# Performance work log

Hardware: AMD Instinct MI355X
Metric: run time of the kernel (lower is better)

## Reference

```python
import jax, jax.numpy as jnp
import numpy as np

WS = (7, 7, 7)          # window size (S, H, W)
NUM_HEADS = 6
DIM = 192
B_, NW = 128, 32        # total windows, windows per image (mask dim)
N = WS[0] * WS[1] * WS[2]  # 343 tokens per window


def _relative_position_index():
    # Faithful replica of the torch __init__ logic (incl. indexing='xy' and
    # the 3*W1-1 / 2*W1-1 multipliers).
    cs = np.arange(WS[0]); ch = np.arange(WS[1]); cw = np.arange(WS[2])
    coords = np.stack(np.meshgrid(cs, ch, cw, indexing='xy'))  # (3, Wh, Ws, Ww)
    cf = coords.reshape(3, -1)                                  # (3, N)
    rel = cf[:, :, None] - cf[:, None, :]                       # (3, N, N)
    rel = rel.transpose(1, 2, 0).astype(np.int64)               # (N, N, 3)
    rel[:, :, 0] += WS[0] - 1
    rel[:, :, 1] += WS[1] - 1
    rel[:, :, 2] += WS[2] - 1
    rel[:, :, 0] *= 3 * WS[1] - 1
    rel[:, :, 1] *= 2 * WS[1] - 1
    return rel.sum(-1)                                          # (N, N) int


def setup_inputs() -> dict:
    key = jax.random.key(0)
    ks = jax.random.split(key, 6)
    C = DIM
    x = jax.random.normal(ks[0], (B_, N, C), dtype=jnp.float32)
    mask = jax.random.normal(ks[1], (NW, N, N), dtype=jnp.float32)
    qkv_w = jax.random.normal(ks[2], (3 * C, C), dtype=jnp.float32) * 0.02
    qkv_b = jnp.zeros((3 * C,), dtype=jnp.float32)
    proj_w = jax.random.normal(ks[3], (C, C), dtype=jnp.float32) * 0.02
    proj_b = jnp.zeros((C,), dtype=jnp.float32)
    table_len = (2 * WS[0] - 1) * (2 * WS[1] - 1) * (2 * WS[2] - 1)
    rpb_table = jax.random.normal(ks[4], (table_len, NUM_HEADS), dtype=jnp.float32) * 0.02
    rel_index = jnp.asarray(_relative_position_index(), dtype=jnp.int32)
    return {"x": x, "mask": mask, "qkv_w": qkv_w, "qkv_b": qkv_b,
            "proj_w": proj_w, "proj_b": proj_b, "rpb_table": rpb_table,
            "rel_index": rel_index}


def reference(x, mask, qkv_w, qkv_b, proj_w, proj_b, rpb_table, rel_index):
    B, n, C = x.shape
    H = NUM_HEADS
    hd = C // H
    scale = hd ** (-0.5)
    qkv = x @ qkv_w.T + qkv_b                      # (B, N, 3C)
    qkv = qkv.reshape(B, n, 3, H, hd).transpose(2, 0, 3, 1, 4)  # (3, B, H, N, hd)
    q, k, v = qkv[0] * scale, qkv[1], qkv[2]
    attn = jnp.einsum('bhnd,bhmd->bhnm', q, k)     # (B, H, N, N)
    bias = rpb_table[rel_index.reshape(-1)].reshape(n, n, H)
    attn = attn + bias.transpose(2, 0, 1)[None]    # (B, H, N, N)
    nW = mask.shape[0]
    attn = attn.reshape(B // nW, nW, H, n, n) + mask[None, :, None]
    attn = jax.nn.softmax(attn.reshape(B, H, n, n), axis=-1)
    out = jnp.einsum('bhnm,bhmd->bhnd', attn, v)   # (B, H, N, hd)
    out = out.transpose(0, 2, 1, 3).reshape(B, n, C)
    return out @ proj_w.T + proj_b
```

## Files before the change

kernel.cpp:

```cpp
#include <hip/hip_runtime.h>
#include <hip/hip_fp16.h>
#include <hip/hip_bf16.h>
#include <stdint.h>

#define WN 343
#define NH 6
#define HD 32
#define CD 192
#define NB 128
#define NWM 32
#define BMROW 352
#define BMSLICE (11*16*BMROW)
#define BMKC (16*BMROW)
#define LOG2E 1.4426950408889634f

typedef __attribute__((ext_vector_type(8))) short short8;
typedef __attribute__((ext_vector_type(4))) float f32x4;

__device__ __forceinline__ unsigned short f2bf(float f) {
  union { float f; uint32_t u; } v; v.f = f;
  uint32_t r = v.u + 0x7fffu + ((v.u >> 16) & 1u);
  return (unsigned short)(r >> 16);
}

__device__ __forceinline__ uint32_t pk2bf(float a, float b) {
  __hip_bfloat162 h = __float22bfloat162_rn(make_float2(a, b));
  return *(uint32_t*)&h;
}

__device__ __forceinline__ uint32_t pkh2(float a, float b) {
  __half2 h; h.x = __float2half(a); h.y = __float2half(b);
  return *(uint32_t*)&h;
}

__global__ __launch_bounds__(256) void prep_kernel(
    const float* __restrict__ wq, const float* __restrict__ wp,
    unsigned short* __restrict__ wqb, unsigned short* __restrict__ wpb,
    const int* __restrict__ rel, const float* __restrict__ rpb,
    const float* __restrict__ mask, uint32_t* __restrict__ bP,
    uint32_t* __restrict__ mP) {
  __shared__ float M[352][33];
  const int bid = blockIdx.x;
  if (bid < 66 + 352) {
    const bool isBias = (bid < 66);
    const int sub = isBias ? bid : bid - 66;
    const int grp = sub / 11;
    const int kc = sub - grp * 11;
    const int k0 = kc * 32;
    const float* mw = mask + (size_t)grp * (WN * WN);
    for (int idx = threadIdx.x; idx < 352 * 32; idx += 256) {
      int n = idx >> 5, k = idx & 31;
      float v;
      if (isBias) {
        int nc = (n < WN) ? n : (WN - 1);
        v = (k0 + k < WN) ? rpb[rel[nc * WN + k0 + k] * NH + grp] * LOG2E
                          : -30000.0f;
      } else {
        v = (n < WN && k0 + k < WN) ? mw[n * WN + k0 + k] * LOG2E : 0.0f;
      }
      M[n][k] = v;
    }
    __syncthreads();
    uint32_t* outp = (isBias ? bP : mP) + (size_t)grp * BMSLICE + (size_t)kc * BMKC;
#pragma unroll
    for (int quad = 0; quad < 4; ++quad) {
#pragma unroll
      for (int j = 0; j < 2; ++j) {
        int n = threadIdx.x + 256 * j;
        if (n < 352) {
          uint4 o;
          o.x = pkh2(M[n][quad * 8 + 0], M[n][quad * 8 + 4]);
          o.y = pkh2(M[n][quad * 8 + 1], M[n][quad * 8 + 5]);
          o.z = pkh2(M[n][quad * 8 + 2], M[n][quad * 8 + 6]);
          o.w = pkh2(M[n][quad * 8 + 3], M[n][quad * 8 + 7]);
          *(uint4*)(outp + ((size_t)quad * 352 + n) * 4) = o;
        }
      }
    }
    return;
  }
  const int NWQ = 3 * CD * CD;
  const int NWP = CD * CD;
  int i4 = ((bid - 418) * 256 + threadIdx.x) * 4;
  const float* src; unsigned short* dst; int off;
  if (i4 < NWQ) { src = wq; dst = wqb; off = i4; }
  else if (i4 < NWQ + NWP) { src = wp; dst = wpb; off = i4 - NWQ; }
  else return;
  f32x4 v = *(const f32x4*)(src + off);
  union { uint2 u2; uint32_t d[2]; } o;
  o.d[0] = pk2bf(v[0], v[1]);
  o.d[1] = pk2bf(v[2], v[3]);
  *(uint2*)(dst + off) = o.u2;
}

__global__ __launch_bounds__(256) void qkv_kernel(
    const float* __restrict__ x, const unsigned short* __restrict__ wqb,
    const float* __restrict__ bvec,
    unsigned short* __restrict__ qb, unsigned short* __restrict__ kb,
    unsigned short* __restrict__ vb) {
  __shared__ __align__(16) unsigned short Xs[128][40];
  __shared__ __align__(16) unsigned short Ws[192][40];
  const int tid = threadIdx.x;
  const int wave = tid >> 6, lane = tid & 63;
  const int quad = lane >> 4, c = lane & 15;
  const int m0 = blockIdx.x * 128;
  const int s = blockIdx.y;
  const int n0 = s * 192;

  f32x4 acc[2][12];
#pragma unroll
  for (int i = 0; i < 2; ++i)
#pragma unroll
    for (int j = 0; j < 12; ++j) acc[i][j] = (f32x4){0.f, 0.f, 0.f, 0.f};

  for (int kt = 0; kt < 6; ++kt) {
    const int k0 = kt * 32;
#pragma unroll
    for (int it = 0; it < 2; ++it) {
      int tq = tid + it * 256;
      int r = tq >> 2, ch = tq & 3;
      const float* src = x + (size_t)(m0 + r) * CD + k0 + ch * 8;
      f32x4 a = *(const f32x4*)src;
      f32x4 b = *(const f32x4*)(src + 4);
      union { short8 v8; uint32_t d[4]; } pk;
      pk.d[0] = pk2bf(a[0], a[1]);
      pk.d[1] = pk2bf(a[2], a[3]);
      pk.d[2] = pk2bf(b[0], b[1]);
      pk.d[3] = pk2bf(b[2], b[3]);
      *(short8*)&Xs[r][ch * 8] = pk.v8;
    }
#pragma unroll
    for (int it = 0; it < 3; ++it) {
      int r = it * 64 + (tid >> 2), ch = tid & 3;
      *(short8*)&Ws[r][ch * 8] =
          *(const short8*)(wqb + (size_t)(n0 + r) * CD + k0 + ch * 8);
    }
    __syncthreads();
    short8 af0 = *(const short8*)&Xs[wave * 32 + c][quad * 8];
    short8 af1 = *(const short8*)&Xs[wave * 32 + 16 + c][quad * 8];
#pragma unroll
    for (int j = 0; j < 12; ++j) {
      short8 bfr = *(const short8*)&Ws[j * 16 + c][quad * 8];
      acc[0][j] = __builtin_amdgcn_mfma_f32_16x16x32_bf16(af0, bfr, acc[0][j], 0, 0, 0);
      acc[1][j] = __builtin_amdgcn_mfma_f32_16x16x32_bf16(af1, bfr, acc[1][j], 0, 0, 0);
    }
    __syncthreads();
  }

  const float qscale = 0.25503486f;
  unsigned short* dst = (s == 0) ? qb : ((s == 1) ? kb : vb);
  const float scl = (s == 0) ? qscale : 1.0f;
  unsigned short (*Lh0)[40] = (unsigned short (*)[40])&Xs[0][0];
  unsigned short (*Lh1)[40] = (unsigned short (*)[40])&Ws[0][0];
  for (int hh = 0; hh < 3; ++hh) {
    __syncthreads();
#pragma unroll
    for (int jj = 0; jj < 4; ++jj) {
      int j = hh * 4 + jj;
      int hl = jj >> 1;
      int dd = (jj & 1) * 16 + c;
      float bn = bvec[n0 + j * 16 + c];
      unsigned short (*L)[40] = hl ? Lh1 : Lh0;
#pragma unroll
      for (int i = 0; i < 2; ++i)
#pragma unroll
        for (int r = 0; r < 4; ++r) {
          int m = wave * 32 + i * 16 + quad * 4 + r;
          L[m][dd] = f2bf((acc[i][j][r] + bn) * scl);
        }
    }
    __syncthreads();
    const int m = tid & 127;
    const int hl = tid >> 7;
    const int M = m0 + m;
    const int b = M / WN;
    const int tok = M - b * WN;
    const int h = hh * 2 + hl;
    unsigned short (*L)[40] = hl ? Lh1 : Lh0;
    unsigned short* drow = dst + (((size_t)b * NH + h) * WN + tok) * HD;
#pragma unroll
    for (int t2 = 0; t2 < 4; ++t2) {
      int d0 = t2 * 8;
      *(short8*)&drow[d0] = *(const short8*)&L[m][d0];
    }
  }
}

__global__ __launch_bounds__(512) void attn_kernel(
    const unsigned short* __restrict__ qb, const unsigned short* __restrict__ kb,
    const unsigned short* __restrict__ vb, const uint32_t* __restrict__ biasP,
    const uint32_t* __restrict__ maskP, unsigned short* __restrict__ ob) {
  __shared__ __align__(16) unsigned short Ks[352][40];
  __shared__ __align__(16) unsigned short Vt[HD][360];
  const int bid = blockIdx.x;
  const int job = (bid & 7) * 96 + (bid >> 3);
  const int wdx = job / 24;
  const int inner = job - wdx * 24;
  const int h = inner >> 2;
  const int b = (inner & 3) * 32 + wdx;
  const int tid = threadIdx.x;
  const int wave = tid >> 6, lane = tid & 63;
  const int quad = lane >> 4, c = lane & 15;
  const size_t base = ((size_t)b * NH + h) * (WN * HD);
  const unsigned short* q = qb + base;
  const unsigned short* k = kb + base;
  const unsigned short* v = vb + base;
  const uint32_t* bP = biasP + (size_t)h * BMSLICE;
  const uint32_t* mP = maskP + (size_t)wdx * BMSLICE;

  for (int t = tid; t < WN * 4; t += 512) {
    int r = t >> 2, ch = t & 3;
    int kk = r & 31;
    int row = (r & ~31) + 16 * ((kk >> 2) & 1) + 4 * (kk >> 3) + (kk & 3);
    *(short8*)&Ks[row][ch * 8] = *(const short8*)(k + r * HD + ch * 8);
  }
  for (int t = tid; t < 9 * 32; t += 512) {
    int kg = WN + (t >> 5);
    int kk = kg & 31;
    int row = (kg & ~31) + 16 * ((kk >> 2) & 1) + 4 * (kk >> 3) + (kk & 3);
    Ks[row][t & 31] = 0;
  }
  for (int t = tid; t < WN; t += 512) {
#pragma unroll
    for (int ch = 0; ch < 4; ++ch) {
      short8 vv = *(const short8*)(v + t * HD + ch * 8);
#pragma unroll
      for (int j = 0; j < 8; ++j) Vt[ch * 8 + j][t] = vv[j];
    }
  }
  for (int t = tid; t < 9 * 32; t += 512) {
    Vt[t & 31][WN + (t >> 5)] = 0;
  }
  __syncthreads();

  for (int qt = wave; qt < 22; qt += 8) {
    const int q0 = qt * 16;
    int qr = q0 + c; if (qr > WN - 1) qr = WN - 1;
    const short8 qf = *(const short8*)(q + qr * HD + quad * 8);
    const uint32_t* bRow = bP + ((size_t)quad * 352 + q0 + c) * 4;
    const uint32_t* mRow = mP + ((size_t)quad * 352 + q0 + c) * 4;

    f32x4 o0 = (f32x4){0.f, 0.f, 0.f, 0.f}, o1 = (f32x4){0.f, 0.f, 0.f, 0.f};
    float l = 0.f;
#pragma unroll
    for (int kc = 0; kc < 11; ++kc) {
      uint4 bw4 = *(const uint4*)(bRow + (size_t)kc * BMKC);
      uint4 mw4 = *(const uint4*)(mRow + (size_t)kc * BMKC);
      f32x4 cc0, cc1;
      {
        __half2 s2; float2 f;
        s2 = __hadd2(*(__half2*)&bw4.x, *(__half2*)&mw4.x);
        f = __half22float2(s2); cc0[0] = f.x; cc1[0] = f.y;
        s2 = __hadd2(*(__half2*)&bw4.y, *(__half2*)&mw4.y);
        f = __half22float2(s2); cc0[1] = f.x; cc1[1] = f.y;
        s2 = __hadd2(*(__half2*)&bw4.z, *(__half2*)&mw4.z);
        f = __half22float2(s2); cc0[2] = f.x; cc1[2] = f.y;
        s2 = __hadd2(*(__half2*)&bw4.w, *(__half2*)&mw4.w);
        f = __half22float2(s2); cc0[3] = f.x; cc1[3] = f.y;
      }
      const int k0 = kc * 32;
      short8 kf0 = *(const short8*)&Ks[k0 + c][quad * 8];
      short8 kf1 = *(const short8*)&Ks[k0 + 16 + c][quad * 8];
      f32x4 s0 = __builtin_amdgcn_mfma_f32_16x16x32_bf16(kf0, qf, cc0, 0, 0, 0);
      f32x4 s1 = __builtin_amdgcn_mfma_f32_16x16x32_bf16(kf1, qf, cc1, 0, 0, 0);
      float p0 = __builtin_amdgcn_exp2f(s0[0]), p1 = __builtin_amdgcn_exp2f(s0[1]);
      float p2 = __builtin_amdgcn_exp2f(s0[2]), p3 = __builtin_amdgcn_exp2f(s0[3]);
      float p4 = __builtin_amdgcn_exp2f(s1[0]), p5 = __builtin_amdgcn_exp2f(s1[1]);
      float p6 = __builtin_amdgcn_exp2f(s1[2]), p7 = __builtin_amdgcn_exp2f(s1[3]);
      l += (p0 + p1 + p2 + p3) + (p4 + p5 + p6 + p7);
      union { short8 v8; uint32_t d[4]; } pf;
      pf.d[0] = pk2bf(p0, p1);
      pf.d[1] = pk2bf(p2, p3);
      pf.d[2] = pk2bf(p4, p5);
      pf.d[3] = pk2bf(p6, p7);
      short8 vf0 = *(const short8*)&Vt[c][k0 + quad * 8];
      short8 vf1 = *(const short8*)&Vt[16 + c][k0 + quad * 8];
      o0 = __builtin_amdgcn_mfma_f32_16x16x32_bf16(pf.v8, vf0, o0, 0, 0, 0);
      o1 = __builtin_amdgcn_mfma_f32_16x16x32_bf16(pf.v8, vf1, o1, 0, 0, 0);
    }
    l += __shfl_xor(l, 16);
    l += __shfl_xor(l, 32);

#pragma unroll
    for (int r = 0; r < 4; ++r) {
      int n = q0 + quad * 4 + r;
      if (n < WN) {
        float lq = __shfl(l, quad * 4 + r, 16);
        float inv = 1.0f / lq;
        size_t orow = ((size_t)b * WN + n) * CD + h * HD;
        ob[orow + c] = f2bf(o0[r] * inv);
        ob[orow + 16 + c] = f2bf(o1[r] * inv);
      }
    }
  }
}

__global__ __launch_bounds__(256) void proj_kernel(
    const unsigned short* __restrict__ ob, const unsigned short* __restrict__ wpb,
    const float* __restrict__ bvec, float* __restrict__ out) {
  __shared__ __align__(16) unsigned short Xs[64][40];
  __shared__ __align__(16) unsigned short Ws[192][40];
  const int tid = threadIdx.x;
  const int wave = tid >> 6, lane = tid & 63;
  const int quad = lane >> 4, c = lane & 15;
  const int m0 = blockIdx.x * 64;

  f32x4 acc[12];
#pragma unroll
  for (int j = 0; j < 12; ++j) acc[j] = (f32x4){0.f, 0.f, 0.f, 0.f};

  for (int kt = 0; kt < 6; ++kt) {
    const int k0 = kt * 32;
    {
      int r = tid >> 2, ch = tid & 3;
      *(short8*)&Xs[r][ch * 8] =
          *(const short8*)(ob + (size_t)(m0 + r) * CD + k0 + ch * 8);
    }
#pragma unroll
    for (int it = 0; it < 3; ++it) {
      int r = it * 64 + (tid >> 2), ch = tid & 3;
      *(short8*)&Ws[r][ch * 8] =
          *(const short8*)(wpb + (size_t)r * CD + k0 + ch * 8);
    }
    __syncthreads();
    short8 af = *(const short8*)&Xs[wave * 16 + c][quad * 8];
#pragma unroll
    for (int j = 0; j < 12; ++j) {
      short8 bfr = *(const short8*)&Ws[j * 16 + c][quad * 8];
      acc[j] = __builtin_amdgcn_mfma_f32_16x16x32_bf16(af, bfr, acc[j], 0, 0, 0);
    }
    __syncthreads();
  }

#pragma unroll
  for (int j = 0; j < 12; ++j) {
    int col = j * 16 + c;
    float bn = bvec[col];
#pragma unroll
    for (int r = 0; r < 4; ++r) {
      int m = m0 + wave * 16 + quad * 4 + r;
      out[(size_t)m * CD + col] = acc[j][r] + bn;
    }
  }
}

extern "C" void kernel_launch(void* const* d_in, const int* in_sizes, int n_in,
                              void* d_out, int out_size, void* d_ws, size_t ws_size,
                              hipStream_t stream) {
  const float* x      = (const float*)d_in[0];
  const float* mask   = (const float*)d_in[1];
  const float* qkv_w  = (const float*)d_in[2];
  const float* qkv_b  = (const float*)d_in[3];
  const float* proj_w = (const float*)d_in[4];
  const float* proj_b = (const float*)d_in[5];
  const float* rpb    = (const float*)d_in[6];
  const int*   rel    = (const int*)d_in[7];
  float* out = (float*)d_out;

  char* ws = (char*)d_ws;
  uint32_t* biasP = (uint32_t*)ws;
  size_t off = 1486848;
  uint32_t* maskP = (uint32_t*)(ws + off); off += 7929856;
  unsigned short* qb = (unsigned short*)(ws + off); off += 16859136;
  unsigned short* kb = (unsigned short*)(ws + off); off += 16859136;
  unsigned short* vb = (unsigned short*)(ws + off); off += 16859136;
  unsigned short* obuf = (unsigned short*)(ws + off); off += 16859136;
  unsigned short* wqb = (unsigned short*)(ws + off); off += 221184;
  unsigned short* wpb = (unsigned short*)(ws + off); off += 73728;

  hipLaunchKernelGGL(prep_kernel, dim3(418 + 144), dim3(256), 0, stream,
                     qkv_w, proj_w, wqb, wpb, rel, rpb, mask, biasP, maskP);
  hipLaunchKernelGGL(qkv_kernel, dim3(343, 3), dim3(256), 0, stream,
                     x, wqb, qkv_b, qb, kb, vb);
  hipLaunchKernelGGL(attn_kernel, dim3(NH * NB), dim3(512), 0, stream,
                     qb, kb, vb, biasP, maskP, obuf);
  hipLaunchKernelGGL(proj_kernel, dim3(686), dim3(256), 0, stream,
                     obuf, wpb, proj_b, out);
}
```

Measured before the change: 219.8 us.

## Stage full activation rows in LDS and stream weights from global in QKV/proj GEMMs

The QKV kernel now uses 64-row tiles. It loads and converts each tile's full 192-column slice of x to bf16 in LDS once, then loops over all three Q/K/V outputs inside one block. Before, x was reread and reconverted for each of three grid-y slices. Both QKV and projection kernels now read weight fragments directly from global memory (relying on cache) instead of staging them in LDS, which removes the per-k-step syncthreads. The cost is more global or L2 weight traffic per block, and a serial 3-way loop per block with smaller row tiles.

Measured after the change: 287.0 us. 1.31x slower.

```diff
diff --git a/kernel.cpp b/kernel.cpp
--- a/kernel.cpp
+++ b/kernel.cpp
@@ -98,90 +98,75 @@
     const float* __restrict__ bvec,
     unsigned short* __restrict__ qb, unsigned short* __restrict__ kb,
     unsigned short* __restrict__ vb) {
-  __shared__ __align__(16) unsigned short Xs[128][40];
-  __shared__ __align__(16) unsigned short Ws[192][40];
+  __shared__ __align__(16) unsigned short Xall[64][200];
+  __shared__ __align__(16) unsigned short Lh0[64][40];
+  __shared__ __align__(16) unsigned short Lh1[64][40];
   const int tid = threadIdx.x;
   const int wave = tid >> 6, lane = tid & 63;
   const int quad = lane >> 4, c = lane & 15;
-  const int m0 = blockIdx.x * 128;
-  const int s = blockIdx.y;
-  const int n0 = s * 192;
-
-  f32x4 acc[2][12];
-#pragma unroll
-  for (int i = 0; i < 2; ++i)
-#pragma unroll
-    for (int j = 0; j < 12; ++j) acc[i][j] = (f32x4){0.f, 0.f, 0.f, 0.f};
-
-  for (int kt = 0; kt < 6; ++kt) {
-    const int k0 = kt * 32;
-#pragma unroll
-    for (int it = 0; it < 2; ++it) {
-      int tq = tid + it * 256;
-      int r = tq >> 2, ch = tq & 3;
-      const float* src = x + (size_t)(m0 + r) * CD + k0 + ch * 8;
-      f32x4 a = *(const f32x4*)src;
-      f32x4 b = *(const f32x4*)(src + 4);
-      union { short8 v8; uint32_t d[4]; } pk;
-      pk.d[0] = pk2bf(a[0], a[1]);
-      pk.d[1] = pk2bf(a[2], a[3]);
-      pk.d[2] = pk2bf(b[0], b[1]);
-      pk.d[3] = pk2bf(b[2], b[3]);
-      *(short8*)&Xs[r][ch * 8] = pk.v8;
-    }
-#pragma unroll
-    for (int it = 0; it < 3; ++it) {
-      int r = it * 64 + (tid >> 2), ch = tid & 3;
-      *(short8*)&Ws[r][ch * 8] =
-          *(const short8*)(wqb + (size_t)(n0 + r) * CD + k0 + ch * 8);
-    }
-    __syncthreads();
-    short8 af0 = *(const short8*)&Xs[wave * 32 + c][quad * 8];
-    short8 af1 = *(const short8*)&Xs[wave * 32 + 16 + c][quad * 8];
-#pragma unroll
-    for (int j = 0; j < 12; ++j) {
-      short8 bfr = *(const short8*)&Ws[j * 16 + c][quad * 8];
-      acc[0][j] = __builtin_amdgcn_mfma_f32_16x16x32_bf16(af0, bfr, acc[0][j], 0, 0, 0);
-      acc[1][j] = __builtin_amdgcn_mfma_f32_16x16x32_bf16(af1, bfr, acc[1][j], 0, 0, 0);
-    }
-    __syncthreads();
-  }
+  const int m0 = blockIdx.x * 64;
+
+#pragma unroll
+  for (int it = 0; it < 6; ++it) {
+    int u = tid + 256 * it;
+    int r = u / 24, c8 = (u - r * 24) * 8;
+    const float* src = x + (size_t)(m0 + r) * CD + c8;
+    f32x4 a = *(const f32x4*)src;
+    f32x4 b = *(const f32x4*)(src + 4);
+    union { short8 v8; uint32_t d[4]; } pk;
+    pk.d[0] = pk2bf(a[0], a[1]);
+    pk.d[1] = pk2bf(a[2], a[3]);
+    pk.d[2] = pk2bf(b[0], b[1]);
+    pk.d[3] = pk2bf(b[2], b[3]);
+    *(short8*)&Xall[r][c8] = pk.v8;
+  }
+  __syncthreads();
 
   const float qscale = 0.25503486f;
-  unsigned short* dst = (s == 0) ? qb : ((s == 1) ? kb : vb);
-  const float scl = (s == 0) ? qscale : 1.0f;
-  unsigned short (*Lh0)[40] = (unsigned short (*)[40])&Xs[0][0];
-  unsigned short (*Lh1)[40] = (unsigned short (*)[40])&Ws[0][0];
-  for (int hh = 0; hh < 3; ++hh) {
-    __syncthreads();
-#pragma unroll
-    for (int jj = 0; jj < 4; ++jj) {
-      int j = hh * 4 + jj;
-      int hl = jj >> 1;
-      int dd = (jj & 1) * 16 + c;
-      float bn = bvec[n0 + j * 16 + c];
+  for (int s = 0; s < 3; ++s) {
+    f32x4 acc[12];
+#pragma unroll
+    for (int j = 0; j < 12; ++j) acc[j] = (f32x4){0.f, 0.f, 0.f, 0.f};
+    const unsigned short* wb = wqb + (size_t)(s * 192 + c) * CD + quad * 8;
+#pragma unroll
+    for (int kt = 0; kt < 6; ++kt) {
+      short8 af = *(const short8*)&Xall[wave * 16 + c][kt * 32 + quad * 8];
+#pragma unroll
+      for (int j = 0; j < 12; ++j) {
+        short8 bfr = *(const short8*)(wb + (size_t)(j * 16) * CD + kt * 32);
+        acc[j] = __builtin_amdgcn_mfma_f32_16x16x32_bf16(af, bfr, acc[j], 0, 0, 0);
+      }
+    }
+    unsigned short* dst = (s == 0) ? qb : ((s == 1) ? kb : vb);
+    const float scl = (s == 0) ? qscale : 1.0f;
+    const int n0 = s * 192;
+    for (int hh = 0; hh < 3; ++hh) {
+      __syncthreads();
+#pragma unroll
+      for (int jj = 0; jj < 4; ++jj) {
+        int j = hh * 4 + jj;
+        int hl = jj >> 1;
+        int dd = (jj & 1) * 16 + c;
+        float bn = bvec[n0 + j * 16 + c];
+        unsigned short (*L)[40] = hl ? Lh1 : Lh0;
+#pragma unroll
+        for (int r = 0; r < 4; ++r) {
+          int m = wave * 16 + quad * 4 + r;
+          L[m][dd] = f2bf((acc[j][r] + bn) * scl);
+        }
+      }
+      __syncthreads();
+      const int m = tid & 63;
+      const int hl = (tid >> 6) & 1;
+      const int half = tid >> 7;
+      const int M = m0 + m;
+      const int b = M / WN;
+      const int tok = M - b * WN;
+      const int h = hh * 2 + hl;
       unsigned short (*L)[40] = hl ? Lh1 : Lh0;
-#pragma unroll
-      for (int i = 0; i < 2; ++i)
-#pragma unroll
-        for (int r = 0; r < 4; ++r) {
-          int m = wave * 32 + i * 16 + quad * 4 + r;
-          L[m][dd] = f2bf((acc[i][j][r] + bn) * scl);
-        }
-    }
-    __syncthreads();
-    const int m = tid & 127;
-    const int hl = tid >> 7;
-    const int M = m0 + m;
-    const int b = M / WN;
-    const int tok = M - b * WN;
-    const int h = hh * 2 + hl;
-    unsigned short (*L)[40] = hl ? Lh1 : Lh0;
-    unsigned short* drow = dst + (((size_t)b * NH + h) * WN + tok) * HD;
-#pragma unroll
-    for (int t2 = 0; t2 < 4; ++t2) {
-      int d0 = t2 * 8;
-      *(short8*)&drow[d0] = *(const short8*)&L[m][d0];
+      unsigned short* drow = dst + (((size_t)b * NH + h) * WN + tok) * HD + half * 16;
+      *(short8*)&drow[0] = *(const short8*)&L[m][half * 16];
+      *(short8*)&drow[8] = *(const short8*)&L[m][half * 16 + 8];
     }
   }
 }
@@ -298,38 +283,32 @@
 __global__ __launch_bounds__(256) void proj_kernel(
     const unsigned short* __restrict__ ob, const unsigned short* __restrict__ wpb,
     const float* __restrict__ bvec, float* __restrict__ out) {
-  __shared__ __align__(16) unsigned short Xs[64][40];
-  __shared__ __align__(16) unsigned short Ws[192][40];
+  __shared__ __align__(16) unsigned short Xall[64][200];
   const int tid = threadIdx.x;
   const int wave = tid >> 6, lane = tid & 63;
   const int quad = lane >> 4, c = lane & 15;
   const int m0 = blockIdx.x * 64;
 
+#pragma unroll
+  for (int it = 0; it < 6; ++it) {
+    int u = tid + 256 * it;
+    int r = u / 24, c8 = (u - r * 24) * 8;
+    *(short8*)&Xall[r][c8] = *(const short8*)(ob + (size_t)(m0 + r) * CD + c8);
+  }
+  __syncthreads();
+
   f32x4 acc[12];
 #pragma unroll
   for (int j = 0; j < 12; ++j) acc[j] = (f32x4){0.f, 0.f, 0.f, 0.f};
-
+  const unsigned short* wb = wpb + (size_t)c * CD + quad * 8;
+#pragma unroll
   for (int kt = 0; kt < 6; ++kt) {
-    const int k0 = kt * 32;
-    {
-      int r = tid >> 2, ch = tid & 3;
-      *(short8*)&Xs[r][ch * 8] =
-          *(const short8*)(ob + (size_t)(m0 + r) * CD + k0 + ch * 8);
-    }
-#pragma unroll
-    for (int it = 0; it < 3; ++it) {
-      int r = it * 64 + (tid >> 2), ch = tid & 3;
-      *(short8*)&Ws[r][ch * 8] =
-          *(const short8*)(wpb + (size_t)r * CD + k0 + ch * 8);
-    }
-    __syncthreads();
-    short8 af = *(const short8*)&Xs[wave * 16 + c][quad * 8];
+    short8 af = *(const short8*)&Xall[wave * 16 + c][kt * 32 + quad * 8];
 #pragma unroll
     for (int j = 0; j < 12; ++j) {
-      short8 bfr = *(const short8*)&Ws[j * 16 + c][quad * 8];
+      short8 bfr = *(const short8*)(wb + (size_t)(j * 16) * CD + kt * 32);
       acc[j] = __builtin_amdgcn_mfma_f32_16x16x32_bf16(af, bfr, acc[j], 0, 0, 0);
     }
-    __syncthreads();
   }
 
 #pragma unroll
@@ -370,7 +349,7 @@
 
   hipLaunchKernelGGL(prep_kernel, dim3(418 + 144), dim3(256), 0, stream,
                      qkv_w, proj_w, wqb, wpb, rel, rpb, mask, biasP, maskP);
-  hipLaunchKernelGGL(qkv_kernel, dim3(343, 3), dim3(256), 0, stream,
+  hipLaunchKernelGGL(qkv_kernel, dim3(686), dim3(256), 0, stream,
                      x, wqb, qkv_b, qb, kb, vb);
   hipLaunchKernelGGL(attn_kernel, dim3(NH * NB), dim3(512), 0, stream,
                      qb, kb, vb, biasP, maskP, obuf);
```

## Pre-convert x to tiled swizzled bf16 and load QKV tiles via global_load_lds

Applied to the files above, without the earlier changes.

The fp32-to-bf16 conversion of x moves out of the QKV GEMM into the prep kernel. x and the QKV weights are written in a tiled, XOR-swizzled layout so the GEMM can stream each k-tile directly into LDS with global_load_lds, avoiding register staging and reducing bank conflicts. This drops the per-block conversion, which was repeated three times (once per Q/K/V slice). The cost is an extra bf16 copy of x written and read through the workspace, plus a larger prep launch.

Measured after the change: 220.0 us. About the same (+0.1%).

```diff
diff --git a/kernel.cpp b/kernel.cpp
--- a/kernel.cpp
+++ b/kernel.cpp
@@ -33,14 +33,22 @@
   return *(uint32_t*)&h;
 }
 
+typedef const __attribute__((address_space(1))) unsigned int* gas_ptr;
+typedef __attribute__((address_space(3))) unsigned int* las_ptr;
+__device__ __forceinline__ void gload16(const unsigned short* g, unsigned short* l) {
+  __builtin_amdgcn_global_load_lds((gas_ptr)(const void*)g, (las_ptr)(void*)l, 16, 0, 0);
+}
+
 __global__ __launch_bounds__(256) void prep_kernel(
     const float* __restrict__ wq, const float* __restrict__ wp,
     unsigned short* __restrict__ wqb, unsigned short* __restrict__ wpb,
     const int* __restrict__ rel, const float* __restrict__ rpb,
     const float* __restrict__ mask, uint32_t* __restrict__ bP,
-    uint32_t* __restrict__ mP) {
+    uint32_t* __restrict__ mP, const float* __restrict__ x,
+    unsigned short* __restrict__ xb) {
   __shared__ float M[352][33];
   const int bid = blockIdx.x;
+  const int tid = threadIdx.x;
   if (bid < 66 + 352) {
     const bool isBias = (bid < 66);
     const int sub = isBias ? bid : bid - 66;
@@ -48,7 +56,7 @@
     const int kc = sub - grp * 11;
     const int k0 = kc * 32;
     const float* mw = mask + (size_t)grp * (WN * WN);
-    for (int idx = threadIdx.x; idx < 352 * 32; idx += 256) {
+    for (int idx = tid; idx < 352 * 32; idx += 256) {
       int n = idx >> 5, k = idx & 31;
       float v;
       if (isBias) {
@@ -66,7 +74,7 @@
     for (int quad = 0; quad < 4; ++quad) {
 #pragma unroll
       for (int j = 0; j < 2; ++j) {
-        int n = threadIdx.x + 256 * j;
+        int n = tid + 256 * j;
         if (n < 352) {
           uint4 o;
           o.x = pkh2(M[n][quad * 8 + 0], M[n][quad * 8 + 4]);
@@ -79,33 +87,65 @@
     }
     return;
   }
-  const int NWQ = 3 * CD * CD;
-  const int NWP = CD * CD;
-  int i4 = ((bid - 418) * 256 + threadIdx.x) * 4;
-  const float* src; unsigned short* dst; int off;
-  if (i4 < NWQ) { src = wq; dst = wqb; off = i4; }
-  else if (i4 < NWQ + NWP) { src = wp; dst = wpb; off = i4 - NWQ; }
-  else return;
-  f32x4 v = *(const f32x4*)(src + off);
-  union { uint2 u2; uint32_t d[2]; } o;
-  o.d[0] = pk2bf(v[0], v[1]);
-  o.d[1] = pk2bf(v[2], v[3]);
-  *(uint2*)(dst + off) = o.u2;
+  int cb = bid - 418;
+  if (cb < 54) {
+    int g = cb * 256 + tid;
+    int sk = g / 768; int rem = g - sk * 768;
+    int row = rem >> 2; int cc = rem & 3;
+    int s = sk / 6; int kt = sk - s * 6;
+    int lch = cc ^ ((row >> 1) & 3);
+    const float* src = wq + (size_t)(s * 192 + row) * CD + kt * 32 + lch * 8;
+    f32x4 a = *(const f32x4*)src;
+    f32x4 b = *(const f32x4*)(src + 4);
+    union { short8 v8; uint32_t d[4]; } pk;
+    pk.d[0] = pk2bf(a[0], a[1]);
+    pk.d[1] = pk2bf(a[2], a[3]);
+    pk.d[2] = pk2bf(b[0], b[1]);
+    pk.d[3] = pk2bf(b[2], b[3]);
+    *(short8*)(wqb + (size_t)g * 8) = pk.v8;
+    return;
+  }
+  cb -= 54;
+  if (cb < 36) {
+    int i4 = (cb * 256 + tid) * 4;
+    f32x4 v = *(const f32x4*)(wp + i4);
+    union { uint2 u2; uint32_t d[2]; } o;
+    o.d[0] = pk2bf(v[0], v[1]);
+    o.d[1] = pk2bf(v[2], v[3]);
+    *(uint2*)(wpb + i4) = o.u2;
+    return;
+  }
+  cb -= 36;
+  size_t gx = (size_t)cb * 256 + tid;
+  int tile = (int)(gx >> 9); int rem = (int)(gx & 511);
+  int row = rem >> 2; int cc = rem & 3;
+  int mb = tile / 6; int kt = tile - mb * 6;
+  int lch = cc ^ ((row >> 1) & 3);
+  const float* src = x + ((size_t)mb * 128 + row) * CD + kt * 32 + lch * 8;
+  f32x4 a = *(const f32x4*)src;
+  f32x4 b = *(const f32x4*)(src + 4);
+  union { short8 v8; uint32_t d[4]; } pk;
+  pk.d[0] = pk2bf(a[0], a[1]);
+  pk.d[1] = pk2bf(a[2], a[3]);
+  pk.d[2] = pk2bf(b[0], b[1]);
+  pk.d[3] = pk2bf(b[2], b[3]);
+  *(short8*)(xb + gx * 8) = pk.v8;
 }
 
 __global__ __launch_bounds__(256) void qkv_kernel(
-    const float* __restrict__ x, const unsigned short* __restrict__ wqb,
+    const unsigned short* __restrict__ xb, const unsigned short* __restrict__ wqb,
     const float* __restrict__ bvec,
     unsigned short* __restrict__ qb, unsigned short* __restrict__ kb,
     unsigned short* __restrict__ vb) {
-  __shared__ __align__(16) unsigned short Xs[128][40];
-  __shared__ __align__(16) unsigned short Ws[192][40];
+  __shared__ __align__(16) unsigned short SL[10240];
+  unsigned short* XL = SL;
+  unsigned short* WL = SL + 4096;
   const int tid = threadIdx.x;
   const int wave = tid >> 6, lane = tid & 63;
   const int quad = lane >> 4, c = lane & 15;
   const int m0 = blockIdx.x * 128;
   const int s = blockIdx.y;
-  const int n0 = s * 192;
+  const int chk = (quad ^ ((c >> 1) & 3)) * 8;
 
   f32x4 acc[2][12];
 #pragma unroll
@@ -113,34 +153,24 @@
 #pragma unroll
     for (int j = 0; j < 12; ++j) acc[i][j] = (f32x4){0.f, 0.f, 0.f, 0.f};
 
+  const size_t xt0 = (size_t)blockIdx.x * 6;
+  const size_t wt0 = (size_t)s * 6;
   for (int kt = 0; kt < 6; ++kt) {
-    const int k0 = kt * 32;
-#pragma unroll
-    for (int it = 0; it < 2; ++it) {
-      int tq = tid + it * 256;
-      int r = tq >> 2, ch = tq & 3;
-      const float* src = x + (size_t)(m0 + r) * CD + k0 + ch * 8;
-      f32x4 a = *(const f32x4*)src;
-      f32x4 b = *(const f32x4*)(src + 4);
-      union { short8 v8; uint32_t d[4]; } pk;
-      pk.d[0] = pk2bf(a[0], a[1]);
-      pk.d[1] = pk2bf(a[2], a[3]);
-      pk.d[2] = pk2bf(b[0], b[1]);
-      pk.d[3] = pk2bf(b[2], b[3]);
-      *(short8*)&Xs[r][ch * 8] = pk.v8;
-    }
-#pragma unroll
-    for (int it = 0; it < 3; ++it) {
-      int r = it * 64 + (tid >> 2), ch = tid & 3;
-      *(short8*)&Ws[r][ch * 8] =
-          *(const short8*)(wqb + (size_t)(n0 + r) * CD + k0 + ch * 8);
-    }
-    __syncthreads();
-    short8 af0 = *(const short8*)&Xs[wave * 32 + c][quad * 8];
-    short8 af1 = *(const short8*)&Xs[wave * 32 + 16 + c][quad * 8];
+    const unsigned short* gx = xb + ((xt0 + kt) << 12) + tid * 8;
+    const unsigned short* gw = wqb + (wt0 + kt) * 6144 + tid * 8;
+    unsigned short* lx = XL + (size_t)wave * 512;
+    unsigned short* lw = WL + (size_t)wave * 512;
+    gload16(gx, lx);
+    gload16(gx + 2048, lx + 2048);
+    gload16(gw, lw);
+    gload16(gw + 2048, lw + 2048);
+    gload16(gw + 4096, lw + 4096);
+    __syncthreads();
+    short8 af0 = *(const short8*)&XL[(wave * 32 + c) * 32 + chk];
+    short8 af1 = *(const short8*)&XL[(wave * 32 + 16 + c) * 32 + chk];
 #pragma unroll
     for (int j = 0; j < 12; ++j) {
-      short8 bfr = *(const short8*)&Ws[j * 16 + c][quad * 8];
+      short8 bfr = *(const short8*)&WL[(j * 16 + c) * 32 + chk];
       acc[0][j] = __builtin_amdgcn_mfma_f32_16x16x32_bf16(af0, bfr, acc[0][j], 0, 0, 0);
       acc[1][j] = __builtin_amdgcn_mfma_f32_16x16x32_bf16(af1, bfr, acc[1][j], 0, 0, 0);
     }
@@ -150,8 +180,9 @@
   const float qscale = 0.25503486f;
   unsigned short* dst = (s == 0) ? qb : ((s == 1) ? kb : vb);
   const float scl = (s == 0) ? qscale : 1.0f;
-  unsigned short (*Lh0)[40] = (unsigned short (*)[40])&Xs[0][0];
-  unsigned short (*Lh1)[40] = (unsigned short (*)[40])&Ws[0][0];
+  const int n0 = s * 192;
+  unsigned short* Lh0 = SL;
+  unsigned short* Lh1 = SL + 4608;
   for (int hh = 0; hh < 3; ++hh) {
     __syncthreads();
 #pragma unroll
@@ -160,13 +191,13 @@
       int hl = jj >> 1;
       int dd = (jj & 1) * 16 + c;
       float bn = bvec[n0 + j * 16 + c];
-      unsigned short (*L)[40] = hl ? Lh1 : Lh0;
+      unsigned short* L = hl ? Lh1 : Lh0;
 #pragma unroll
       for (int i = 0; i < 2; ++i)
 #pragma unroll
         for (int r = 0; r < 4; ++r) {
           int m = wave * 32 + i * 16 + quad * 4 + r;
-          L[m][dd] = f2bf((acc[i][j][r] + bn) * scl);
+          L[m * 36 + dd] = f2bf((acc[i][j][r] + bn) * scl);
         }
     }
     __syncthreads();
@@ -176,12 +207,12 @@
     const int b = M / WN;
     const int tok = M - b * WN;
     const int h = hh * 2 + hl;
-    unsigned short (*L)[40] = hl ? Lh1 : Lh0;
+    const unsigned short* L = hl ? Lh1 : Lh0;
     unsigned short* drow = dst + (((size_t)b * NH + h) * WN + tok) * HD;
 #pragma unroll
     for (int t2 = 0; t2 < 4; ++t2) {
       int d0 = t2 * 8;
-      *(short8*)&drow[d0] = *(const short8*)&L[m][d0];
+      *(short8*)&drow[d0] = *(const short8*)&L[m * 36 + d0];
     }
   }
 }
@@ -367,11 +398,12 @@
   unsigned short* obuf = (unsigned short*)(ws + off); off += 16859136;
   unsigned short* wqb = (unsigned short*)(ws + off); off += 221184;
   unsigned short* wpb = (unsigned short*)(ws + off); off += 73728;
-
-  hipLaunchKernelGGL(prep_kernel, dim3(418 + 144), dim3(256), 0, stream,
-                     qkv_w, proj_w, wqb, wpb, rel, rpb, mask, biasP, maskP);
+  unsigned short* xb  = (unsigned short*)(ws + off); off += 16859136;
+
+  hipLaunchKernelGGL(prep_kernel, dim3(418 + 54 + 36 + 4116), dim3(256), 0, stream,
+                     qkv_w, proj_w, wqb, wpb, rel, rpb, mask, biasP, maskP, x, xb);
   hipLaunchKernelGGL(qkv_kernel, dim3(343, 3), dim3(256), 0, stream,
-                     x, wqb, qkv_b, qb, kb, vb);
+                     xb, wqb, qkv_b, qb, kb, vb);
   hipLaunchKernelGGL(attn_kernel, dim3(NH * NB), dim3(512), 0, stream,
                      qb, kb, vb, biasP, maskP, obuf);
   hipLaunchKernelGGL(proj_kernel, dim3(686), dim3(256), 0, stream,
```
